# Performance work log

Measured on AMD Instinct MI355X. Metric: run time of the kernel, lower is better.

Reference implementation:

```python
import jax, jax.numpy as jnp
import numpy as np

N_NODES = 100000
N_EDGES = 500000
E_HIDDEN = 64
R_HIDDEN = 32
N_RELS = 500
EPS = 1e-16


def setup_inputs() -> dict:
    key = jax.random.key(0)
    k1, k2, k3, k4, k5 = jax.random.split(key, 5)
    x = jax.random.normal(k1, (N_NODES, E_HIDDEN), dtype=jnp.float32)
    edge_index_all = jax.random.randint(k2, (2, N_EDGES), 0, N_NODES, dtype=jnp.int32)
    rel_all = jax.random.randint(k3, (N_EDGES,), 0, N_RELS, dtype=jnp.int32)
    rel_emb = jax.random.normal(k4, (N_RELS, R_HIDDEN), dtype=jnp.float32)
    ww_weight = jax.random.normal(k5, (2 * E_HIDDEN + R_HIDDEN,), dtype=jnp.float32) * 0.05
    return {"x": x, "edge_index_all": edge_index_all, "rel_all": rel_all,
            "rel_emb": rel_emb, "ww_weight": ww_weight}


def reference(x, edge_index_all, rel_all, rel_emb, ww_weight):
    n = x.shape[0]
    ei = edge_index_all[0]  # destination / group index
    ej = edge_index_all[1]
    # gather per-edge features: [E, 2*e_hidden + r_hidden]
    feats = jnp.concatenate([x[ei], rel_emb[rel_all], x[ej]], axis=1)
    # linear attention score (Linear(d, 1, bias=False)) -> [E]
    att = feats @ ww_weight
    # segment softmax grouped by ei (numerically stable)
    seg_max = jax.ops.segment_max(att, ei, num_segments=n)
    att = jnp.exp(att - seg_max[ei])
    seg_sum = jax.ops.segment_sum(att, ei, num_segments=n)
    att = att / (seg_sum[ei] + EPS)
    # weighted scatter-sum aggregate -> [N, 2*e_hidden + r_hidden]
    x_e = jax.ops.segment_sum(feats * att[:, None], ei, num_segments=n)
    e_features = jax.nn.relu(x_e)
    return jnp.concatenate([x, e_features], axis=1)
```

## Files before the change

kernel.cpp:

```cpp
#include <hip/hip_runtime.h>
#include <math.h>

#define N_NODES 100000
#define N_EDGES 500000
#define E_HID   64
#define R_HID   32
#define N_RELS  500
#define D_OUT   224
#define EPSF    1e-16f

#define SRC_BITS 17
#define SRC_MASK ((1 << SRC_BITS) - 1)
#define CAP      32
#define CAP_SH   5

typedef float v4f __attribute__((ext_vector_type(4)));
typedef float v2f __attribute__((ext_vector_type(2)));
typedef int   v4i __attribute__((ext_vector_type(4)));

__device__ __forceinline__ void nt_store4(float* p, float a, float b, float c, float d) {
    v4f v = {a, b, c, d};
    __builtin_nontemporal_store(v, (v4f*)p);
}
__device__ __forceinline__ void nt_store2(float* p, float a, float b) {
    v2f v = {a, b};
    __builtin_nontemporal_store(v, (v2f*)p);
}

__device__ __forceinline__ float dot4(float4 a, float4 b) {
    return a.x * b.x + a.y * b.y + a.z * b.z + a.w * b.w;
}
__device__ __forceinline__ float4 axpy4(float s, float4 a, float4 acc) {
    acc.x += s * a.x; acc.y += s * a.y; acc.z += s * a.z; acc.w += s * a.w;
    return acc;
}
__device__ __forceinline__ float qreduce16(float v) {
    v += __shfl_xor(v, 1, 16);
    v += __shfl_xor(v, 2, 16);
    v += __shfl_xor(v, 4, 16);
    v += __shfl_xor(v, 8, 16);
    return v;
}

__global__ __launch_bounds__(256) void scatter_kernel(const int* __restrict__ ei,
                                                      const int* __restrict__ ej,
                                                      const int* __restrict__ rel,
                                                      int* __restrict__ cnt,
                                                      int* __restrict__ slots) {
    int i = blockIdx.x * 256 + threadIdx.x;
    if (i >= N_EDGES / 4) return;
    v4i d4 = __builtin_nontemporal_load((const v4i*)ei + i);
    v4i s4 = __builtin_nontemporal_load((const v4i*)ej + i);
    v4i r4 = __builtin_nontemporal_load((const v4i*)rel + i);
    int pos;
    pos = atomicAdd(&cnt[d4.x], 1);
    if (pos < CAP) slots[(d4.x << CAP_SH) + pos] = s4.x | (r4.x << SRC_BITS);
    pos = atomicAdd(&cnt[d4.y], 1);
    if (pos < CAP) slots[(d4.y << CAP_SH) + pos] = s4.y | (r4.y << SRC_BITS);
    pos = atomicAdd(&cnt[d4.z], 1);
    if (pos < CAP) slots[(d4.z << CAP_SH) + pos] = s4.z | (r4.z << SRC_BITS);
    pos = atomicAdd(&cnt[d4.w], 1);
    if (pos < CAP) slots[(d4.w << CAP_SH) + pos] = s4.w | (r4.w << SRC_BITS);
}

__global__ __launch_bounds__(256) void aggregate_kernel(const int* __restrict__ slots,
                                                        const int* __restrict__ cnt,
                                                        const float* __restrict__ x,
                                                        const float* __restrict__ rel_emb,
                                                        const float* __restrict__ ww,
                                                        float* __restrict__ out) {
    int t    = blockIdx.x * 256 + threadIdx.x;
    int node = t >> 4;
    int sub  = t & 15;

    const float4* xb = (const float4*)x;
    const float2* rb = (const float2*)rel_emb;

    const int* sl = slots + (node << CAP_SH);
    int4   p       = *(const int4*)sl;
    int    c       = cnt[node];
    float4 xv_self = xb[(node << 4) + sub];

    float4 wb = *(const float4*)&ww[96 + sub * 4];
    float2 wr = *(const float2*)&ww[64 + sub * 2];

    c = (c < CAP) ? c : CAP;

    float  S    = 0.0f;
    float4 accx = make_float4(0.f, 0.f, 0.f, 0.f);
    float2 accr = make_float2(0.f, 0.f);

    for (int k = 0; k < c; k += 4) {
        int4 pn = *(const int4*)&sl[k + 4];
        int  m  = c - k;
        int s0 = p.x & SRC_MASK, r0 = (unsigned)p.x >> SRC_BITS;
        int s1 = p.y & SRC_MASK, r1 = (unsigned)p.y >> SRC_BITS;
        int s2 = p.z & SRC_MASK, r2 = (unsigned)p.z >> SRC_BITS;
        int s3 = p.w & SRC_MASK, r3 = (unsigned)p.w >> SRC_BITS;
        if (m < 2) { s1 = 0; r1 = 0; }
        if (m < 3) { s2 = 0; r2 = 0; }
        if (m < 4) { s3 = 0; r3 = 0; }
        float4 x0 = xb[(s0 << 4) + sub];
        float4 x1 = xb[(s1 << 4) + sub];
        float4 x2 = xb[(s2 << 4) + sub];
        float4 x3 = xb[(s3 << 4) + sub];
        float2 e0 = rb[(r0 << 4) + sub];
        float2 e1 = rb[(r1 << 4) + sub];
        float2 e2 = rb[(r2 << 4) + sub];
        float2 e3 = rb[(r3 << 4) + sub];
        float d0 = dot4(x0, wb) + e0.x * wr.x + e0.y * wr.y;
        float d1 = dot4(x1, wb) + e1.x * wr.x + e1.y * wr.y;
        float d2 = dot4(x2, wb) + e2.x * wr.x + e2.y * wr.y;
        float d3 = dot4(x3, wb) + e3.x * wr.x + e3.y * wr.y;
        d0 = qreduce16(d0);
        d1 = qreduce16(d1);
        d2 = qreduce16(d2);
        d3 = qreduce16(d3);
        float se0 = __expf(d0);
        float se1 = (m > 1) ? __expf(d1) : 0.f;
        float se2 = (m > 2) ? __expf(d2) : 0.f;
        float se3 = (m > 3) ? __expf(d3) : 0.f;
        S += (se0 + se1) + (se2 + se3);
        accx = axpy4(se0, x0, accx); accx = axpy4(se1, x1, accx);
        accx = axpy4(se2, x2, accx); accx = axpy4(se3, x3, accx);
        accr.x += se0 * e0.x + se1 * e1.x + se2 * e2.x + se3 * e3.x;
        accr.y += se0 * e0.y + se1 * e1.y + se2 * e2.y + se3 * e3.y;
        p = pn;
    }

    float wv    = 1.0f / (S + EPSF);
    float alpha = S * wv;
    float* o = out + (size_t)node * D_OUT;
    nt_store4(&o[sub * 4], xv_self.x, xv_self.y, xv_self.z, xv_self.w);
    nt_store4(&o[64 + sub * 4],
              fmaxf(alpha * xv_self.x, 0.f), fmaxf(alpha * xv_self.y, 0.f),
              fmaxf(alpha * xv_self.z, 0.f), fmaxf(alpha * xv_self.w, 0.f));
    nt_store2(&o[128 + sub * 2],
              fmaxf(accr.x * wv, 0.f), fmaxf(accr.y * wv, 0.f));
    nt_store4(&o[160 + sub * 4],
              fmaxf(accx.x * wv, 0.f), fmaxf(accx.y * wv, 0.f),
              fmaxf(accx.z * wv, 0.f), fmaxf(accx.w * wv, 0.f));
}

extern "C" void kernel_launch(void* const* d_in, const int* in_sizes, int n_in,
                              void* d_out, int out_size, void* d_ws, size_t ws_size,
                              hipStream_t stream) {
    const float* x        = (const float*)d_in[0];
    const int*   edge_all = (const int*)  d_in[1];
    const int*   rel      = (const int*)  d_in[2];
    const float* rel_emb  = (const float*)d_in[3];
    const float* ww       = (const float*)d_in[4];
    float*       out      = (float*)d_out;

    const int* ei = edge_all;
    const int* ej = edge_all + N_EDGES;

    int* cnt   = (int*)d_ws;
    int* slots = cnt + N_NODES;

    (void)hipMemsetAsync(cnt, 0, (size_t)N_NODES * sizeof(int), stream);
    scatter_kernel<<<(N_EDGES / 4 + 255) / 256, 256, 0, stream>>>(ei, ej, rel, cnt, slots);
    aggregate_kernel<<<(N_NODES * 16) / 256, 256, 0, stream>>>(slots, cnt, x, rel_emb, ww, out);
}
```

Baseline: 173.0 us.

## Precompute per-node and per-relation scores, store edge exp weights in slots

Adds a pre-pass kernel that computes the x·w_j score per node and the rel_emb·w_r score per relation, and also zeroes the count array in place of the memset. The scatter kernel now computes each edge's exp weight from these scalars and stores it with the packed source and relation in an int2 slot. The aggregate kernel therefore drops its per-edge dot products, shuffle reductions and exps. The cost is one extra kernel launch, slot storage twice as large, and two extra random scalar gathers per edge in scatter.

```diff
diff --git a/kernel.cpp b/kernel.cpp
--- a/kernel.cpp
+++ b/kernel.cpp
@@ -13,6 +13,10 @@
 #define SRC_MASK ((1 << SRC_BITS) - 1)
 #define CAP      32
 #define CAP_SH   5
+
+#define NSB  ((N_NODES * 16) / 256)
+#define RSB  ((N_RELS * 8 + 255) / 256)
+#define PRE_GRID (NSB + RSB)
 
 typedef float v4f __attribute__((ext_vector_type(4)));
 typedef float v2f __attribute__((ext_vector_type(2)));
@@ -34,40 +38,68 @@
     acc.x += s * a.x; acc.y += s * a.y; acc.z += s * a.z; acc.w += s * a.w;
     return acc;
 }
-__device__ __forceinline__ float qreduce16(float v) {
-    v += __shfl_xor(v, 1, 16);
-    v += __shfl_xor(v, 2, 16);
-    v += __shfl_xor(v, 4, 16);
-    v += __shfl_xor(v, 8, 16);
-    return v;
+
+__global__ __launch_bounds__(256) void pre_kernel(const float* __restrict__ x,
+                                                  const float* __restrict__ rel_emb,
+                                                  const float* __restrict__ ww,
+                                                  float* __restrict__ s_j,
+                                                  float* __restrict__ s_r,
+                                                  int* __restrict__ cnt) {
+    int b = blockIdx.x;
+    if (b < NSB) {
+        int t    = b * 256 + threadIdx.x;
+        int node = t >> 4, sub = t & 15;
+        float4 v  = *(const float4*)&x[node * E_HID + sub * 4];
+        float4 wb = *(const float4*)&ww[96 + sub * 4];
+        float a = dot4(v, wb);
+        #pragma unroll
+        for (int off = 8; off > 0; off >>= 1) a += __shfl_down(a, off, 16);
+        if (sub == 0) s_j[node] = a;
+        if (t < N_NODES) cnt[t] = 0;
+    } else {
+        int t = (b - NSB) * 256 + threadIdx.x;
+        int r = t >> 3, sub = t & 7;
+        if (r >= N_RELS) return;
+        float4 v  = *(const float4*)&rel_emb[r * R_HID + sub * 4];
+        float4 wr = *(const float4*)&ww[64 + sub * 4];
+        float a = dot4(v, wr);
+        #pragma unroll
+        for (int off = 4; off > 0; off >>= 1) a += __shfl_down(a, off, 8);
+        if (sub == 0) s_r[r] = a;
+    }
 }
 
 __global__ __launch_bounds__(256) void scatter_kernel(const int* __restrict__ ei,
                                                       const int* __restrict__ ej,
                                                       const int* __restrict__ rel,
+                                                      const float* __restrict__ s_j,
+                                                      const float* __restrict__ s_r,
                                                       int* __restrict__ cnt,
-                                                      int* __restrict__ slots) {
+                                                      int2* __restrict__ slots) {
     int i = blockIdx.x * 256 + threadIdx.x;
     if (i >= N_EDGES / 4) return;
     v4i d4 = __builtin_nontemporal_load((const v4i*)ei + i);
     v4i s4 = __builtin_nontemporal_load((const v4i*)ej + i);
     v4i r4 = __builtin_nontemporal_load((const v4i*)rel + i);
+    float se0 = __expf(s_j[s4.x] + s_r[r4.x]);
+    float se1 = __expf(s_j[s4.y] + s_r[r4.y]);
+    float se2 = __expf(s_j[s4.z] + s_r[r4.z]);
+    float se3 = __expf(s_j[s4.w] + s_r[r4.w]);
     int pos;
     pos = atomicAdd(&cnt[d4.x], 1);
-    if (pos < CAP) slots[(d4.x << CAP_SH) + pos] = s4.x | (r4.x << SRC_BITS);
+    if (pos < CAP) slots[(d4.x << CAP_SH) + pos] = make_int2(s4.x | (r4.x << SRC_BITS), __float_as_int(se0));
     pos = atomicAdd(&cnt[d4.y], 1);
-    if (pos < CAP) slots[(d4.y << CAP_SH) + pos] = s4.y | (r4.y << SRC_BITS);
+    if (pos < CAP) slots[(d4.y << CAP_SH) + pos] = make_int2(s4.y | (r4.y << SRC_BITS), __float_as_int(se1));
     pos = atomicAdd(&cnt[d4.z], 1);
-    if (pos < CAP) slots[(d4.z << CAP_SH) + pos] = s4.z | (r4.z << SRC_BITS);
+    if (pos < CAP) slots[(d4.z << CAP_SH) + pos] = make_int2(s4.z | (r4.z << SRC_BITS), __float_as_int(se2));
     pos = atomicAdd(&cnt[d4.w], 1);
-    if (pos < CAP) slots[(d4.w << CAP_SH) + pos] = s4.w | (r4.w << SRC_BITS);
+    if (pos < CAP) slots[(d4.w << CAP_SH) + pos] = make_int2(s4.w | (r4.w << SRC_BITS), __float_as_int(se3));
 }
 
-__global__ __launch_bounds__(256) void aggregate_kernel(const int* __restrict__ slots,
+__global__ __launch_bounds__(256) void aggregate_kernel(const int2* __restrict__ slots,
                                                         const int* __restrict__ cnt,
                                                         const float* __restrict__ x,
                                                         const float* __restrict__ rel_emb,
-                                                        const float* __restrict__ ww,
                                                         float* __restrict__ out) {
     int t    = blockIdx.x * 256 + threadIdx.x;
     int node = t >> 4;
@@ -76,13 +108,11 @@
     const float4* xb = (const float4*)x;
     const float2* rb = (const float2*)rel_emb;
 
-    const int* sl = slots + (node << CAP_SH);
-    int4   p       = *(const int4*)sl;
+    const int4* sl = (const int4*)(slots + (node << CAP_SH));
+    int4   pa      = sl[0];
+    int4   pb      = sl[1];
     int    c       = cnt[node];
     float4 xv_self = xb[(node << 4) + sub];
-
-    float4 wb = *(const float4*)&ww[96 + sub * 4];
-    float2 wr = *(const float2*)&ww[64 + sub * 2];
 
     c = (c < CAP) ? c : CAP;
 
@@ -91,12 +121,17 @@
     float2 accr = make_float2(0.f, 0.f);
 
     for (int k = 0; k < c; k += 4) {
-        int4 pn = *(const int4*)&sl[k + 4];
+        int4 na = sl[(k >> 1) + 2];
+        int4 nb = sl[(k >> 1) + 3];
         int  m  = c - k;
-        int s0 = p.x & SRC_MASK, r0 = (unsigned)p.x >> SRC_BITS;
-        int s1 = p.y & SRC_MASK, r1 = (unsigned)p.y >> SRC_BITS;
-        int s2 = p.z & SRC_MASK, r2 = (unsigned)p.z >> SRC_BITS;
-        int s3 = p.w & SRC_MASK, r3 = (unsigned)p.w >> SRC_BITS;
+        int s0 = pa.x & SRC_MASK, r0 = (unsigned)pa.x >> SRC_BITS;
+        int s1 = pa.z & SRC_MASK, r1 = (unsigned)pa.z >> SRC_BITS;
+        int s2 = pb.x & SRC_MASK, r2 = (unsigned)pb.x >> SRC_BITS;
+        int s3 = pb.z & SRC_MASK, r3 = (unsigned)pb.z >> SRC_BITS;
+        float se0 = __int_as_float(pa.y);
+        float se1 = (m > 1) ? __int_as_float(pa.w) : 0.f;
+        float se2 = (m > 2) ? __int_as_float(pb.y) : 0.f;
+        float se3 = (m > 3) ? __int_as_float(pb.w) : 0.f;
         if (m < 2) { s1 = 0; r1 = 0; }
         if (m < 3) { s2 = 0; r2 = 0; }
         if (m < 4) { s3 = 0; r3 = 0; }
@@ -108,24 +143,12 @@
         float2 e1 = rb[(r1 << 4) + sub];
         float2 e2 = rb[(r2 << 4) + sub];
         float2 e3 = rb[(r3 << 4) + sub];
-        float d0 = dot4(x0, wb) + e0.x * wr.x + e0.y * wr.y;
-        float d1 = dot4(x1, wb) + e1.x * wr.x + e1.y * wr.y;
-        float d2 = dot4(x2, wb) + e2.x * wr.x + e2.y * wr.y;
-        float d3 = dot4(x3, wb) + e3.x * wr.x + e3.y * wr.y;
-        d0 = qreduce16(d0);
-        d1 = qreduce16(d1);
-        d2 = qreduce16(d2);
-        d3 = qreduce16(d3);
-        float se0 = __expf(d0);
-        float se1 = (m > 1) ? __expf(d1) : 0.f;
-        float se2 = (m > 2) ? __expf(d2) : 0.f;
-        float se3 = (m > 3) ? __expf(d3) : 0.f;
         S += (se0 + se1) + (se2 + se3);
         accx = axpy4(se0, x0, accx); accx = axpy4(se1, x1, accx);
         accx = axpy4(se2, x2, accx); accx = axpy4(se3, x3, accx);
         accr.x += se0 * e0.x + se1 * e1.x + se2 * e2.x + se3 * e3.x;
         accr.y += se0 * e0.y + se1 * e1.y + se2 * e2.y + se3 * e3.y;
-        p = pn;
+        pa = na; pb = nb;
     }
 
     float wv    = 1.0f / (S + EPSF);
@@ -155,10 +178,13 @@
     const int* ei = edge_all;
     const int* ej = edge_all + N_EDGES;
 
-    int* cnt   = (int*)d_ws;
-    int* slots = cnt + N_NODES;
+    int*   cnt   = (int*)d_ws;
+    float* s_j   = (float*)(cnt + N_NODES);
+    float* s_r   = s_j + N_NODES;
+    int2*  slots = (int2*)(s_r + 512);
 
-    (void)hipMemsetAsync(cnt, 0, (size_t)N_NODES * sizeof(int), stream);
-    scatter_kernel<<<(N_EDGES / 4 + 255) / 256, 256, 0, stream>>>(ei, ej, rel, cnt, slots);
-    aggregate_kernel<<<(N_NODES * 16) / 256, 256, 0, stream>>>(slots, cnt, x, rel_emb, ww, out);
+    pre_kernel<<<PRE_GRID, 256, 0, stream>>>(x, rel_emb, ww, s_j, s_r, cnt);
+    scatter_kernel<<<(N_EDGES / 4 + 255) / 256, 256, 0, stream>>>(ei, ej, rel,
+                                                                  s_j, s_r, cnt, slots);
+    aggregate_kernel<<<(N_NODES * 16) / 256, 256, 0, stream>>>(slots, cnt, x, rel_emb, out);
 }
```

Result: slower. 178.6 us (+3.2%).
